# Kernel optimization log

Hardware: AMD Instinct MI355X
Metric: run time of the kernel (lower is better)

The kernel has to match this reference:

```python
import jax, jax.numpy as jnp
import numpy as np

R, S, V, F = 4096, 128, 3, 35  # n_rays, n_samples, n_views(=3 fixed by rgb_fc), in_feat_ch+3


def _kaiming(key, fan_out, fan_in):
    return jax.random.normal(key, (fan_out, fan_in), jnp.float32) * jnp.sqrt(2.0 / fan_in)


def setup_inputs() -> dict:
    key = jax.random.key(0)
    ks = jax.random.split(key, 8)
    rgb_feat = jax.random.normal(ks[0], (R, S, V, F), jnp.float32)
    # base_fc: 105 -> 64 -> 32
    bw1, bw2 = _kaiming(ks[1], 64, 105), _kaiming(ks[2], 32, 64)
    # vis_fc: 32 -> 32 -> 32
    vw1, vw2 = _kaiming(ks[3], 32, 32), _kaiming(ks[4], 32, 32)
    # rgb_fc: 96 -> 32 -> 16 -> 3
    rw1, rw2, rw3 = _kaiming(ks[5], 32, 96), _kaiming(ks[6], 16, 32), _kaiming(ks[7], 3, 16)
    z = jnp.zeros
    return {
        "rgb_feat": rgb_feat,
        "bw1": bw1, "bb1": z((64,)), "bw2": bw2, "bb2": z((32,)),
        "vw1": vw1, "vb1": z((32,)), "vw2": vw2, "vb2": z((32,)),
        "rw1": rw1, "rb1": z((32,)), "rw2": rw2, "rb2": z((16,)), "rw3": rw3, "rb3": z((3,)),
    }


def _lin(x, w, b):
    return x @ w.T + b


def reference(rgb_feat, bw1, bb1, bw2, bb2, vw1, vb1, vw2, vb2,
              rw1, rb1, rw2, rb2, rw3, rb3):
    elu = jax.nn.elu
    num_views = rgb_feat.shape[2]
    rgb_in = rgb_feat[..., :3]
    # fused mean/variance over the views axis (dim=2)
    mean = jnp.mean(rgb_feat, axis=2, keepdims=True)          # [R,S,1,F]
    var = jnp.mean((rgb_feat - mean) ** 2, axis=2, keepdims=True)
    globalfeat = jnp.concatenate([mean, var], axis=-1)         # [R,S,1,2F]
    x = jnp.concatenate(
        [jnp.broadcast_to(globalfeat, (rgb_feat.shape[0], rgb_feat.shape[1], num_views, globalfeat.shape[-1])),
         rgb_feat], axis=-1)                                   # [R,S,V,3F]
    x = elu(_lin(elu(_lin(x, bw1, bb1)), bw2, bb2))            # [R,S,V,32]
    x_vis = elu(_lin(elu(_lin(x / num_views, vw1, vb1)), vw2, vb2))
    x = x + x_vis
    h = x.reshape(x.shape[0], x.shape[1], num_views * 32)      # [R,S,96]
    rgb_out = jax.nn.sigmoid(_lin(elu(_lin(elu(_lin(h, rw1, rb1)), rw2, rb2)), rw3, rb3))
    return (rgb_in, rgb_out)
```

## Files before the change

kernel.cpp:

```cpp
#include <hip/hip_runtime.h>
#include <hip/hip_bf16.h>

#define NPTS      524288
#define OUT2_BASE 4718592

using bf16x8 = __attribute__((ext_vector_type(8))) short;
using f32x4  = __attribute__((ext_vector_type(4))) float;


__device__ __forceinline__ ushort f2bf(float f) {
    union { float f; unsigned u; } v; v.f = f;
    unsigned u = v.u;
    unsigned r = u + 0x7fffu + ((u >> 16) & 1u);
    return (ushort)(r >> 16);
}
__device__ __forceinline__ uint pack2(float a, float b) {
    union { __hip_bfloat162 h; uint u; } cv;
    cv.h = __float22bfloat162_rn(make_float2(a, b));
    return cv.u;
}
__device__ __forceinline__ float eluf(float x) {
    return fmaxf(x, 0.f) + __expf(fminf(x, 0.f)) - 1.f;
}
__device__ __forceinline__ float sigm(float x) { return 1.f / (1.f + __expf(-x)); }

__device__ __forceinline__ void load8(const float* __restrict__ p, float* d) {
    __builtin_memcpy(d, p, 16);
    __builtin_memcpy(d + 4, p + 4, 16);
}

__global__ void prep_k(const float* __restrict__ bw1, const float* __restrict__ bw2,
                       const float* __restrict__ vw1, const float* __restrict__ vw2,
                       const float* __restrict__ rw1, const float* __restrict__ rw2,
                       ushort* __restrict__ w)
{
    int i = blockIdx.x * 256 + threadIdx.x;
    if (i < 6144) {
        int n = i / 96, k = i % 96;
        float val = 0.f;
        if (k < 35)                 val = bw1[n * 105 + k];
        else if (k >= 40 && k < 75) val = bw1[n * 105 + 35 + (k - 40)];
        w[i] = f2bf(val);
    } else if (i < 10752) {
        int t = i - 6144, n = t / 72, k = t % 72;
        w[i] = f2bf(k < 35 ? bw1[n * 105 + 70 + k] : 0.f);
    } else if (i < 13056) {
        int t = i - 10752, n = t / 72, k = t % 72;
        w[i] = f2bf(k < 64 ? bw2[n * 64 + k] : 0.f);
    } else if (i < 14336) {
        int t = i - 13056, n = t / 40, k = t % 40;
        w[i] = f2bf(k < 32 ? vw1[n * 32 + k] * (1.f / 3.f) : 0.f);
    } else if (i < 15616) {
        int t = i - 14336, n = t / 40, k = t % 40;
        w[i] = f2bf(k < 32 ? vw2[n * 32 + k] : 0.f);
    } else if (i < 18944) {
        int t = i - 15616, n = t / 104, k = t % 104;
        w[i] = f2bf(k < 96 ? rw1[n * 96 + k] : 0.f);
    } else if (i < 19584) {
        int t = i - 18944, n = t / 40, k = t % 40;
        w[i] = f2bf(k < 32 ? rw2[n * 32 + k] : 0.f);
    }
}

__global__ __launch_bounds__(128, 4) void mlp_k(
    const float* __restrict__ feat, const ushort* __restrict__ w,
    const float* __restrict__ bb1, const float* __restrict__ bb2,
    const float* __restrict__ vb1, const float* __restrict__ vb2,
    const float* __restrict__ rb1, const float* __restrict__ rb2,
    const float* __restrict__ rw3, const float* __restrict__ rb3,
    float* __restrict__ out)
{
    __shared__ __align__(16) ushort shA[3456];
    __shared__ __align__(16) ushort shB[1664];
    __shared__ __align__(16) ushort shC[3456];

    const int tid  = threadIdx.x;
    const int wv   = tid >> 6;
    const int lane = tid & 63;
    const int n16  = lane & 15;
    const int quad = lane >> 4;
    const long long pbase = (long long)blockIdx.x * 16;

    const ushort* WG = w;
    const ushort* WF = w + 6144;
    const ushort* W2 = w + 10752;
    const ushort* V1 = w + 13056;
    const ushort* V2 = w + 14336;
    const ushort* R1 = w + 15616;
    const ushort* R2 = w + 18944;

    float bb1v[2];
#pragma unroll
    for (int ntl = 0; ntl < 2; ++ntl) bb1v[ntl] = bb1[(wv * 2 + ntl) * 16 + n16];
    const float bb2v = bb2[wv * 16 + n16];
    const float vb1v = vb1[wv * 16 + n16];
    const float vb2v = vb2[wv * 16 + n16];
    const float rb1v = rb1[wv * 16 + n16];
    const float rb2v = rb2[n16];

    {
        const uint4 z = make_uint4(0u, 0u, 0u, 0u);
        uint4* zc = (uint4*)shC;
        for (int i = tid; i < 144; i += 128) {
            int r = i / 3, c = i - r * 3;
            zc[r * 9 + 5 + c] = z;
        }
        if (tid < 32) {
            uint4* zb = (uint4*)shB;
            int r = tid >> 1, c = tid & 1;
            zb[r * 12 + 10 + c] = z;
        }
        for (int i = tid; i < 144; i += 128) {
            int p = i / 9, r = i - p * 9, v = r / 3, c = r - v * 3;
            out[pbase * 9 + i] = feat[(pbase + p) * 105 + v * 35 + c];
        }
        if (tid < 80) {
            int p  = tid / 5;
            int g  = tid - p * 5;
            int k8 = g * 8;
            const float* row = feat + (pbase + p) * 105;
            float X0[8], X1[8], X2[8];
            load8(row + k8,      X0);
            load8(row + 35 + k8, X1);
            if (k8 == 32 && (pbase + p) == (long long)NPTS - 1) {
                X2[0] = row[102]; X2[1] = row[103]; X2[2] = row[104];
                X2[3] = 0.f; X2[4] = 0.f; X2[5] = 0.f; X2[6] = 0.f; X2[7] = 0.f;
            } else {
                load8(row + 70 + k8, X2);
            }
            float M[8], VV[8];
#pragma unroll
            for (int j = 0; j < 8; ++j) {
                float a = X0[j], b = X1[j], c = X2[j];
                float m  = (a + b + c) * (1.f / 3.f);
                float da = a - m, db = b - m, dc = c - m;
                M[j]  = m;
                VV[j] = (da * da + db * db + dc * dc) * (1.f / 3.f);
            }
            *(uint4*)(shC + p * 72 + k8) =
                make_uint4(pack2(X0[0], X0[1]), pack2(X0[2], X0[3]),
                           pack2(X0[4], X0[5]), pack2(X0[6], X0[7]));
            *(uint4*)(shC + (16 + p) * 72 + k8) =
                make_uint4(pack2(X1[0], X1[1]), pack2(X1[2], X1[3]),
                           pack2(X1[4], X1[5]), pack2(X1[6], X1[7]));
            *(uint4*)(shC + (32 + p) * 72 + k8) =
                make_uint4(pack2(X2[0], X2[1]), pack2(X2[2], X2[3]),
                           pack2(X2[4], X2[5]), pack2(X2[6], X2[7]));
            *(uint4*)(shB + p * 96 + k8) =
                make_uint4(pack2(M[0], M[1]), pack2(M[2], M[3]),
                           pack2(M[4], M[5]), pack2(M[6], M[7]));
            *(uint4*)(shB + p * 96 + 40 + k8) =
                make_uint4(pack2(VV[0], VV[1]), pack2(VV[2], VV[3]),
                           pack2(VV[4], VV[5]), pack2(VV[6], VV[7]));
        }
    }
    __syncthreads();

    const f32x4 Z = {0.f, 0.f, 0.f, 0.f};

    f32x4 Cg[2]    = {Z, Z};
    f32x4 Cf[3][2] = {{Z, Z}, {Z, Z}, {Z, Z}};
#pragma unroll
    for (int ks = 0; ks < 3; ++ks) {
        bf16x8 a = *(const bf16x8*)(shB + n16 * 96 + ks * 32 + quad * 8);
#pragma unroll
        for (int ntl = 0; ntl < 2; ++ntl) {
            bf16x8 b = *(const bf16x8*)(WG + ((wv * 2 + ntl) * 16 + n16) * 96 + ks * 32 + quad * 8);
            Cg[ntl] = __builtin_amdgcn_mfma_f32_16x16x32_bf16(a, b, Cg[ntl], 0, 0, 0);
        }
    }
#pragma unroll
    for (int ks = 0; ks < 2; ++ks) {
        bf16x8 a0 = *(const bf16x8*)(shC + (0 * 16 + n16) * 72 + ks * 32 + quad * 8);
        bf16x8 a1 = *(const bf16x8*)(shC + (1 * 16 + n16) * 72 + ks * 32 + quad * 8);
        bf16x8 a2 = *(const bf16x8*)(shC + (2 * 16 + n16) * 72 + ks * 32 + quad * 8);
#pragma unroll
        for (int ntl = 0; ntl < 2; ++ntl) {
            bf16x8 b = *(const bf16x8*)(WF + ((wv * 2 + ntl) * 16 + n16) * 72 + ks * 32 + quad * 8);
            Cf[0][ntl] = __builtin_amdgcn_mfma_f32_16x16x32_bf16(a0, b, Cf[0][ntl], 0, 0, 0);
            Cf[1][ntl] = __builtin_amdgcn_mfma_f32_16x16x32_bf16(a1, b, Cf[1][ntl], 0, 0, 0);
            Cf[2][ntl] = __builtin_amdgcn_mfma_f32_16x16x32_bf16(a2, b, Cf[2][ntl], 0, 0, 0);
        }
    }
#pragma unroll
    for (int mt = 0; mt < 3; ++mt)
#pragma unroll
        for (int ntl = 0; ntl < 2; ++ntl) {
            float e0 = eluf(Cf[mt][ntl][0] + Cg[ntl][0] + bb1v[ntl]);
            float e1 = eluf(Cf[mt][ntl][1] + Cg[ntl][1] + bb1v[ntl]);
            float e2 = eluf(Cf[mt][ntl][2] + Cg[ntl][2] + bb1v[ntl]);
            float e3 = eluf(Cf[mt][ntl][3] + Cg[ntl][3] + bb1v[ntl]);
            int col = (wv * 2 + ntl) * 16 + n16;
            int r0  = (mt * 16 + quad * 4) * 72 + col;
            uint u01 = pack2(e0, e1), u23 = pack2(e2, e3);
            shA[r0]           = (ushort)u01;
            shA[r0 + 72]      = (ushort)(u01 >> 16);
            shA[r0 + 144]     = (ushort)u23;
            shA[r0 + 216]     = (ushort)(u23 >> 16);
        }
    __syncthreads();

    f32x4 C2[3] = {Z, Z, Z};
#pragma unroll
    for (int ks = 0; ks < 2; ++ks) {
        bf16x8 a0 = *(const bf16x8*)(shA + (0 * 16 + n16) * 72 + ks * 32 + quad * 8);
        bf16x8 a1 = *(const bf16x8*)(shA + (1 * 16 + n16) * 72 + ks * 32 + quad * 8);
        bf16x8 a2 = *(const bf16x8*)(shA + (2 * 16 + n16) * 72 + ks * 32 + quad * 8);
        bf16x8 b  = *(const bf16x8*)(W2 + (wv * 16 + n16) * 72 + ks * 32 + quad * 8);
        C2[0] = __builtin_amdgcn_mfma_f32_16x16x32_bf16(a0, b, C2[0], 0, 0, 0);
        C2[1] = __builtin_amdgcn_mfma_f32_16x16x32_bf16(a1, b, C2[1], 0, 0, 0);
        C2[2] = __builtin_amdgcn_mfma_f32_16x16x32_bf16(a2, b, C2[2], 0, 0, 0);
    }
    float h2r[3][4];
#pragma unroll
    for (int mt = 0; mt < 3; ++mt) {
        float e0 = eluf(C2[mt][0] + bb2v);
        float e1 = eluf(C2[mt][1] + bb2v);
        float e2 = eluf(C2[mt][2] + bb2v);
        float e3 = eluf(C2[mt][3] + bb2v);
        h2r[mt][0] = e0; h2r[mt][1] = e1; h2r[mt][2] = e2; h2r[mt][3] = e3;
        int r0 = (mt * 16 + quad * 4) * 72 + wv * 16 + n16;
        uint u01 = pack2(e0, e1), u23 = pack2(e2, e3);
        shC[r0]       = (ushort)u01;
        shC[r0 + 72]  = (ushort)(u01 >> 16);
        shC[r0 + 144] = (ushort)u23;
        shC[r0 + 216] = (ushort)(u23 >> 16);
    }
    __syncthreads();

    f32x4 T1[3] = {Z, Z, Z};
    {
        bf16x8 a0 = *(const bf16x8*)(shC + (0 * 16 + n16) * 72 + quad * 8);
        bf16x8 a1 = *(const bf16x8*)(shC + (1 * 16 + n16) * 72 + quad * 8);
        bf16x8 a2 = *(const bf16x8*)(shC + (2 * 16 + n16) * 72 + quad * 8);
        bf16x8 b  = *(const bf16x8*)(V1 + (wv * 16 + n16) * 40 + quad * 8);
        T1[0] = __builtin_amdgcn_mfma_f32_16x16x32_bf16(a0, b, T1[0], 0, 0, 0);
        T1[1] = __builtin_amdgcn_mfma_f32_16x16x32_bf16(a1, b, T1[1], 0, 0, 0);
        T1[2] = __builtin_amdgcn_mfma_f32_16x16x32_bf16(a2, b, T1[2], 0, 0, 0);
    }
#pragma unroll
    for (int mt = 0; mt < 3; ++mt) {
        float e0 = eluf(T1[mt][0] + vb1v);
        float e1 = eluf(T1[mt][1] + vb1v);
        float e2 = eluf(T1[mt][2] + vb1v);
        float e3 = eluf(T1[mt][3] + vb1v);
        int r0 = (mt * 16 + quad * 4) * 72 + wv * 16 + n16;
        uint u01 = pack2(e0, e1), u23 = pack2(e2, e3);
        shA[r0]       = (ushort)u01;
        shA[r0 + 72]  = (ushort)(u01 >> 16);
        shA[r0 + 144] = (ushort)u23;
        shA[r0 + 216] = (ushort)(u23 >> 16);
    }
    __syncthreads();

    f32x4 T2[3] = {Z, Z, Z};
    {
        bf16x8 a0 = *(const bf16x8*)(shA + (0 * 16 + n16) * 72 + quad * 8);
        bf16x8 a1 = *(const bf16x8*)(shA + (1 * 16 + n16) * 72 + quad * 8);
        bf16x8 a2 = *(const bf16x8*)(shA + (2 * 16 + n16) * 72 + quad * 8);
        bf16x8 b  = *(const bf16x8*)(V2 + (wv * 16 + n16) * 40 + quad * 8);
        T2[0] = __builtin_amdgcn_mfma_f32_16x16x32_bf16(a0, b, T2[0], 0, 0, 0);
        T2[1] = __builtin_amdgcn_mfma_f32_16x16x32_bf16(a1, b, T2[1], 0, 0, 0);
        T2[2] = __builtin_amdgcn_mfma_f32_16x16x32_bf16(a2, b, T2[2], 0, 0, 0);
    }
#pragma unroll
    for (int mt = 0; mt < 3; ++mt) {
        float x0  = h2r[mt][0] + eluf(T2[mt][0] + vb2v);
        float x1  = h2r[mt][1] + eluf(T2[mt][1] + vb2v);
        float x2v = h2r[mt][2] + eluf(T2[mt][2] + vb2v);
        float x3  = h2r[mt][3] + eluf(T2[mt][3] + vb2v);
        int col = mt * 32 + wv * 16 + n16;
        int r0  = (quad * 4) * 104 + col;
        uint u01 = pack2(x0, x1), u23 = pack2(x2v, x3);
        shB[r0]       = (ushort)u01;
        shB[r0 + 104] = (ushort)(u01 >> 16);
        shB[r0 + 208] = (ushort)u23;
        shB[r0 + 312] = (ushort)(u23 >> 16);
    }
    __syncthreads();

    f32x4 CR = Z;
#pragma unroll
    for (int ks = 0; ks < 3; ++ks) {
        bf16x8 a = *(const bf16x8*)(shB + n16 * 104 + ks * 32 + quad * 8);
        bf16x8 b = *(const bf16x8*)(R1 + (wv * 16 + n16) * 104 + ks * 32 + quad * 8);
        CR = __builtin_amdgcn_mfma_f32_16x16x32_bf16(a, b, CR, 0, 0, 0);
    }
    {
        float e0 = eluf(CR[0] + rb1v);
        float e1 = eluf(CR[1] + rb1v);
        float e2 = eluf(CR[2] + rb1v);
        float e3 = eluf(CR[3] + rb1v);
        int r0 = (quad * 4) * 40 + wv * 16 + n16;
        uint u01 = pack2(e0, e1), u23 = pack2(e2, e3);
        shC[r0]       = (ushort)u01;
        shC[r0 + 40]  = (ushort)(u01 >> 16);
        shC[r0 + 80]  = (ushort)u23;
        shC[r0 + 120] = (ushort)(u23 >> 16);
    }
    __syncthreads();

    f32x4 C3 = Z;
    {
        bf16x8 a = *(const bf16x8*)(shC + n16 * 40 + quad * 8);
        bf16x8 b = *(const bf16x8*)(R2 + n16 * 40 + quad * 8);
        C3 = __builtin_amdgcn_mfma_f32_16x16x32_bf16(a, b, C3, 0, 0, 0);
    }
    {
        float* r2b = (float*)shA;
#pragma unroll
        for (int rr = 0; rr < 2; ++rr) {
            int r = 2 * wv + rr;
            r2b[(quad * 4 + r) * 20 + n16] = eluf(C3[r] + rb2v);
        }
    }
    __syncthreads();

    if (tid < 48) {
        const float* r2b = (const float*)shA;
        int p = tid / 3, c = tid - p * 3;
        const float4* rr = (const float4*)(r2b + p * 20);
        const float4* w3 = (const float4*)(rw3 + c * 16);
        float4 a0 = rr[0], a1 = rr[1], a2 = rr[2], a3 = rr[3];
        float4 q0 = w3[0], q1 = w3[1], q2 = w3[2], q3 = w3[3];
        float s = rb3[c];
        s += a0.x * q0.x + a0.y * q0.y + a0.z * q0.z + a0.w * q0.w;
        s += a1.x * q1.x + a1.y * q1.y + a1.z * q1.z + a1.w * q1.w;
        s += a2.x * q2.x + a2.y * q2.y + a2.z * q2.z + a2.w * q2.w;
        s += a3.x * q3.x + a3.y * q3.y + a3.z * q3.z + a3.w * q3.w;
        out[OUT2_BASE + pbase * 3 + tid] = sigm(s);
    }
}

extern "C" void kernel_launch(void* const* d_in, const int* in_sizes, int n_in,
                              void* d_out, int out_size, void* d_ws, size_t ws_size,
                              hipStream_t stream) {
    const float* feat = (const float*)d_in[0];
    const float* bw1  = (const float*)d_in[1];
    const float* bb1  = (const float*)d_in[2];
    const float* bw2  = (const float*)d_in[3];
    const float* bb2  = (const float*)d_in[4];
    const float* vw1  = (const float*)d_in[5];
    const float* vb1  = (const float*)d_in[6];
    const float* vw2  = (const float*)d_in[7];
    const float* vb2  = (const float*)d_in[8];
    const float* rw1  = (const float*)d_in[9];
    const float* rb1  = (const float*)d_in[10];
    const float* rw2  = (const float*)d_in[11];
    const float* rb2  = (const float*)d_in[12];
    const float* rw3  = (const float*)d_in[13];
    const float* rb3  = (const float*)d_in[14];
    ushort* w  = (ushort*)d_ws;
    float* out = (float*)d_out;

    hipLaunchKernelGGL(prep_k, dim3(77), dim3(256), 0, stream,
                       bw1, bw2, vw1, vw2, rw1, rw2, w);
    hipLaunchKernelGGL(mlp_k, dim3(NPTS / 16), dim3(128), 0, stream,
                       feat, w, bb1, bb2, vb1, vb2, rb1, rb2, rw3, rb3, out);
}
```

Before: 429.0 us.

## Loop each block over many point tiles with weights held in registers

After: 484.0 us. 1.13x slower.

```diff
diff --git a/kernel.cpp b/kernel.cpp
--- a/kernel.cpp
+++ b/kernel.cpp
@@ -3,6 +3,9 @@
 
 #define NPTS      524288
 #define OUT2_BASE 4718592
+#define NTILES    32768
+#define NBLK      2048
+#define TPB       16
 
 using bf16x8 = __attribute__((ext_vector_type(8))) short;
 using f32x4  = __attribute__((ext_vector_type(4))) float;
@@ -79,7 +82,6 @@
     const int lane = tid & 63;
     const int n16  = lane & 15;
     const int quad = lane >> 4;
-    const long long pbase = (long long)blockIdx.x * 16;
 
     const ushort* WG = w;
     const ushort* WF = w + 6144;
@@ -98,6 +100,50 @@
     const float rb1v = rb1[wv * 16 + n16];
     const float rb2v = rb2[n16];
 
+    bf16x8 WFf[2][2], W2f[2];
+#pragma unroll
+    for (int ks = 0; ks < 2; ++ks) {
+#pragma unroll
+        for (int ntl = 0; ntl < 2; ++ntl)
+            WFf[ks][ntl] = *(const bf16x8*)(WF + ((wv * 2 + ntl) * 16 + n16) * 72 + ks * 32 + quad * 8);
+        W2f[ks] = *(const bf16x8*)(W2 + (wv * 16 + n16) * 72 + ks * 32 + quad * 8);
+    }
+    const bf16x8 V1f = *(const bf16x8*)(V1 + (wv * 16 + n16) * 40 + quad * 8);
+    const bf16x8 V2f = *(const bf16x8*)(V2 + (wv * 16 + n16) * 40 + quad * 8);
+    const bf16x8 R2f = *(const bf16x8*)(R2 + n16 * 40 + quad * 8);
+    const ushort* WGp[2] = { WG + ((wv * 2 + 0) * 16 + n16) * 96 + quad * 8,
+                             WG + ((wv * 2 + 1) * 16 + n16) * 96 + quad * 8 };
+    const ushort* R1p    = R1 + (wv * 16 + n16) * 104 + quad * 8;
+
+    const int c_p = tid / 9, c_r = tid - c_p * 9;
+    const int c_v = c_r / 3, c_c = c_r - c_v * 3;
+    const int cp_in0 = c_p * 105 + c_v * 35 + c_c;
+    const int i2 = tid + 128;
+    const int d_p = i2 / 9, d_r = i2 - d_p * 9;
+    const int d_v = d_r / 3, d_c = d_r - d_v * 3;
+    const int cp_in1 = d_p * 105 + d_v * 35 + d_c;
+
+    const int  bp   = tid / 5;
+    const int  k8   = (tid - bp * 5) * 8;
+    const bool bthr = tid < 80;
+    const bool gthr = bthr && (k8 == 32) && (bp == 15) && (blockIdx.x == NBLK - 1);
+    ushort* const stXf0 = shC + bp * 72 + k8;
+    ushort* const stXf1 = shC + (16 + bp) * 72 + k8;
+    ushort* const stXf2 = shC + (32 + bp) * 72 + k8;
+    ushort* const stXg0 = shB + bp * 96 + k8;
+    ushort* const stXg1 = shB + bp * 96 + 40 + k8;
+
+    const bool fthr = tid < 48;
+    const int  fp = tid / 3, fc = tid - fp * 3;
+    float4 q0 = {0,0,0,0}, q1 = q0, q2 = q0, q3 = q0;
+    float  rb3c = 0.f;
+    if (fthr) {
+        const float4* w3 = (const float4*)(rw3 + fc * 16);
+        q0 = w3[0]; q1 = w3[1]; q2 = w3[2]; q3 = w3[3];
+        rb3c = rb3[fc];
+    }
+    const float* const r2row = (const float*)shA + fp * 20;
+
     {
         const uint4 z = make_uint4(0u, 0u, 0u, 0u);
         uint4* zc = (uint4*)shC;
@@ -110,23 +156,29 @@
             int r = tid >> 1, c = tid & 1;
             zb[r * 12 + 10 + c] = z;
         }
-        for (int i = tid; i < 144; i += 128) {
-            int p = i / 9, r = i - p * 9, v = r / 3, c = r - v * 3;
-            out[pbase * 9 + i] = feat[(pbase + p) * 105 + v * 35 + c];
-        }
-        if (tid < 80) {
-            int p  = tid / 5;
-            int g  = tid - p * 5;
-            int k8 = g * 8;
-            const float* row = feat + (pbase + p) * 105;
+    }
+
+    const long long pbase0 = (long long)blockIdx.x * (TPB * 16);
+    const float* fin  = feat + pbase0 * 105;
+    const float* brow = feat + (pbase0 + bp) * 105;
+    float*       orgb = out + pbase0 * 9;
+    float*       o2   = out + OUT2_BASE + pbase0 * 3;
+
+    const f32x4 Z = {0.f, 0.f, 0.f, 0.f};
+
+#pragma unroll 1
+    for (int it = 0; it < TPB; ++it) {
+        orgb[tid] = fin[cp_in0];
+        if (tid < 16) orgb[i2] = fin[cp_in1];
+        if (bthr) {
             float X0[8], X1[8], X2[8];
-            load8(row + k8,      X0);
-            load8(row + 35 + k8, X1);
-            if (k8 == 32 && (pbase + p) == (long long)NPTS - 1) {
-                X2[0] = row[102]; X2[1] = row[103]; X2[2] = row[104];
+            load8(brow + k8,      X0);
+            load8(brow + 35 + k8, X1);
+            if (gthr && it == TPB - 1) {
+                X2[0] = brow[102]; X2[1] = brow[103]; X2[2] = brow[104];
                 X2[3] = 0.f; X2[4] = 0.f; X2[5] = 0.f; X2[6] = 0.f; X2[7] = 0.f;
             } else {
-                load8(row + 70 + k8, X2);
+                load8(brow + 70 + k8, X2);
             }
             float M[8], VV[8];
 #pragma unroll
@@ -137,198 +189,187 @@
                 M[j]  = m;
                 VV[j] = (da * da + db * db + dc * dc) * (1.f / 3.f);
             }
-            *(uint4*)(shC + p * 72 + k8) =
-                make_uint4(pack2(X0[0], X0[1]), pack2(X0[2], X0[3]),
-                           pack2(X0[4], X0[5]), pack2(X0[6], X0[7]));
-            *(uint4*)(shC + (16 + p) * 72 + k8) =
-                make_uint4(pack2(X1[0], X1[1]), pack2(X1[2], X1[3]),
-                           pack2(X1[4], X1[5]), pack2(X1[6], X1[7]));
-            *(uint4*)(shC + (32 + p) * 72 + k8) =
-                make_uint4(pack2(X2[0], X2[1]), pack2(X2[2], X2[3]),
-                           pack2(X2[4], X2[5]), pack2(X2[6], X2[7]));
-            *(uint4*)(shB + p * 96 + k8) =
-                make_uint4(pack2(M[0], M[1]), pack2(M[2], M[3]),
-                           pack2(M[4], M[5]), pack2(M[6], M[7]));
-            *(uint4*)(shB + p * 96 + 40 + k8) =
-                make_uint4(pack2(VV[0], VV[1]), pack2(VV[2], VV[3]),
-                           pack2(VV[4], VV[5]), pack2(VV[6], VV[7]));
-        }
-    }
-    __syncthreads();
-
-    const f32x4 Z = {0.f, 0.f, 0.f, 0.f};
-
-    f32x4 Cg[2]    = {Z, Z};
-    f32x4 Cf[3][2] = {{Z, Z}, {Z, Z}, {Z, Z}};
-#pragma unroll
-    for (int ks = 0; ks < 3; ++ks) {
-        bf16x8 a = *(const bf16x8*)(shB + n16 * 96 + ks * 32 + quad * 8);
-#pragma unroll
-        for (int ntl = 0; ntl < 2; ++ntl) {
-            bf16x8 b = *(const bf16x8*)(WG + ((wv * 2 + ntl) * 16 + n16) * 96 + ks * 32 + quad * 8);
-            Cg[ntl] = __builtin_amdgcn_mfma_f32_16x16x32_bf16(a, b, Cg[ntl], 0, 0, 0);
-        }
-    }
-#pragma unroll
-    for (int ks = 0; ks < 2; ++ks) {
-        bf16x8 a0 = *(const bf16x8*)(shC + (0 * 16 + n16) * 72 + ks * 32 + quad * 8);
-        bf16x8 a1 = *(const bf16x8*)(shC + (1 * 16 + n16) * 72 + ks * 32 + quad * 8);
-        bf16x8 a2 = *(const bf16x8*)(shC + (2 * 16 + n16) * 72 + ks * 32 + quad * 8);
-#pragma unroll
-        for (int ntl = 0; ntl < 2; ++ntl) {
-            bf16x8 b = *(const bf16x8*)(WF + ((wv * 2 + ntl) * 16 + n16) * 72 + ks * 32 + quad * 8);
-            Cf[0][ntl] = __builtin_amdgcn_mfma_f32_16x16x32_bf16(a0, b, Cf[0][ntl], 0, 0, 0);
-            Cf[1][ntl] = __builtin_amdgcn_mfma_f32_16x16x32_bf16(a1, b, Cf[1][ntl], 0, 0, 0);
-            Cf[2][ntl] = __builtin_amdgcn_mfma_f32_16x16x32_bf16(a2, b, Cf[2][ntl], 0, 0, 0);
-        }
-    }
-#pragma unroll
-    for (int mt = 0; mt < 3; ++mt)
-#pragma unroll
-        for (int ntl = 0; ntl < 2; ++ntl) {
-            float e0 = eluf(Cf[mt][ntl][0] + Cg[ntl][0] + bb1v[ntl]);
-            float e1 = eluf(Cf[mt][ntl][1] + Cg[ntl][1] + bb1v[ntl]);
-            float e2 = eluf(Cf[mt][ntl][2] + Cg[ntl][2] + bb1v[ntl]);
-            float e3 = eluf(Cf[mt][ntl][3] + Cg[ntl][3] + bb1v[ntl]);
-            int col = (wv * 2 + ntl) * 16 + n16;
-            int r0  = (mt * 16 + quad * 4) * 72 + col;
+            *(uint4*)stXf0 = make_uint4(pack2(X0[0], X0[1]), pack2(X0[2], X0[3]),
+                                        pack2(X0[4], X0[5]), pack2(X0[6], X0[7]));
+            *(uint4*)stXf1 = make_uint4(pack2(X1[0], X1[1]), pack2(X1[2], X1[3]),
+                                        pack2(X1[4], X1[5]), pack2(X1[6], X1[7]));
+            *(uint4*)stXf2 = make_uint4(pack2(X2[0], X2[1]), pack2(X2[2], X2[3]),
+                                        pack2(X2[4], X2[5]), pack2(X2[6], X2[7]));
+            *(uint4*)stXg0 = make_uint4(pack2(M[0], M[1]), pack2(M[2], M[3]),
+                                        pack2(M[4], M[5]), pack2(M[6], M[7]));
+            *(uint4*)stXg1 = make_uint4(pack2(VV[0], VV[1]), pack2(VV[2], VV[3]),
+                                        pack2(VV[4], VV[5]), pack2(VV[6], VV[7]));
+        }
+        __syncthreads();
+
+        f32x4 Cg[2]    = {Z, Z};
+        f32x4 Cf[3][2] = {{Z, Z}, {Z, Z}, {Z, Z}};
+#pragma unroll
+        for (int ks = 0; ks < 3; ++ks) {
+            bf16x8 a = *(const bf16x8*)(shB + n16 * 96 + ks * 32 + quad * 8);
+#pragma unroll
+            for (int ntl = 0; ntl < 2; ++ntl) {
+                bf16x8 b = *(const bf16x8*)(WGp[ntl] + ks * 32);
+                Cg[ntl] = __builtin_amdgcn_mfma_f32_16x16x32_bf16(a, b, Cg[ntl], 0, 0, 0);
+            }
+        }
+#pragma unroll
+        for (int ks = 0; ks < 2; ++ks) {
+            bf16x8 a0 = *(const bf16x8*)(shC + (0 * 16 + n16) * 72 + ks * 32 + quad * 8);
+            bf16x8 a1 = *(const bf16x8*)(shC + (1 * 16 + n16) * 72 + ks * 32 + quad * 8);
+            bf16x8 a2 = *(const bf16x8*)(shC + (2 * 16 + n16) * 72 + ks * 32 + quad * 8);
+#pragma unroll
+            for (int ntl = 0; ntl < 2; ++ntl) {
+                Cf[0][ntl] = __builtin_amdgcn_mfma_f32_16x16x32_bf16(a0, WFf[ks][ntl], Cf[0][ntl], 0, 0, 0);
+                Cf[1][ntl] = __builtin_amdgcn_mfma_f32_16x16x32_bf16(a1, WFf[ks][ntl], Cf[1][ntl], 0, 0, 0);
+                Cf[2][ntl] = __builtin_amdgcn_mfma_f32_16x16x32_bf16(a2, WFf[ks][ntl], Cf[2][ntl], 0, 0, 0);
+            }
+        }
+#pragma unroll
+        for (int mt = 0; mt < 3; ++mt)
+#pragma unroll
+            for (int ntl = 0; ntl < 2; ++ntl) {
+                float e0 = eluf(Cf[mt][ntl][0] + Cg[ntl][0] + bb1v[ntl]);
+                float e1 = eluf(Cf[mt][ntl][1] + Cg[ntl][1] + bb1v[ntl]);
+                float e2 = eluf(Cf[mt][ntl][2] + Cg[ntl][2] + bb1v[ntl]);
+                float e3 = eluf(Cf[mt][ntl][3] + Cg[ntl][3] + bb1v[ntl]);
+                int col = (wv * 2 + ntl) * 16 + n16;
+                int r0  = (mt * 16 + quad * 4) * 72 + col;
+                uint u01 = pack2(e0, e1), u23 = pack2(e2, e3);
+                shA[r0]       = (ushort)u01;
+                shA[r0 + 72]  = (ushort)(u01 >> 16);
+                shA[r0 + 144] = (ushort)u23;
+                shA[r0 + 216] = (ushort)(u23 >> 16);
+            }
+        __syncthreads();
+
+        f32x4 C2[3] = {Z, Z, Z};
+#pragma unroll
+        for (int ks = 0; ks < 2; ++ks) {
+            bf16x8 a0 = *(const bf16x8*)(shA + (0 * 16 + n16) * 72 + ks * 32 + quad * 8);
+            bf16x8 a1 = *(const bf16x8*)(shA + (1 * 16 + n16) * 72 + ks * 32 + quad * 8);
+            bf16x8 a2 = *(const bf16x8*)(shA + (2 * 16 + n16) * 72 + ks * 32 + quad * 8);
+            C2[0] = __builtin_amdgcn_mfma_f32_16x16x32_bf16(a0, W2f[ks], C2[0], 0, 0, 0);
+            C2[1] = __builtin_amdgcn_mfma_f32_16x16x32_bf16(a1, W2f[ks], C2[1], 0, 0, 0);
+            C2[2] = __builtin_amdgcn_mfma_f32_16x16x32_bf16(a2, W2f[ks], C2[2], 0, 0, 0);
+        }
+        float h2r[3][4];
+#pragma unroll
+        for (int mt = 0; mt < 3; ++mt) {
+            float e0 = eluf(C2[mt][0] + bb2v);
+            float e1 = eluf(C2[mt][1] + bb2v);
+            float e2 = eluf(C2[mt][2] + bb2v);
+            float e3 = eluf(C2[mt][3] + bb2v);
+            h2r[mt][0] = e0; h2r[mt][1] = e1; h2r[mt][2] = e2; h2r[mt][3] = e3;
+            int r0 = (mt * 16 + quad * 4) * 72 + wv * 16 + n16;
             uint u01 = pack2(e0, e1), u23 = pack2(e2, e3);
-            shA[r0]           = (ushort)u01;
-            shA[r0 + 72]      = (ushort)(u01 >> 16);
-            shA[r0 + 144]     = (ushort)u23;
-            shA[r0 + 216]     = (ushort)(u23 >> 16);
-        }
-    __syncthreads();
-
-    f32x4 C2[3] = {Z, Z, Z};
-#pragma unroll
-    for (int ks = 0; ks < 2; ++ks) {
-        bf16x8 a0 = *(const bf16x8*)(shA + (0 * 16 + n16) * 72 + ks * 32 + quad * 8);
-        bf16x8 a1 = *(const bf16x8*)(shA + (1 * 16 + n16) * 72 + ks * 32 + quad * 8);
-        bf16x8 a2 = *(const bf16x8*)(shA + (2 * 16 + n16) * 72 + ks * 32 + quad * 8);
-        bf16x8 b  = *(const bf16x8*)(W2 + (wv * 16 + n16) * 72 + ks * 32 + quad * 8);
-        C2[0] = __builtin_amdgcn_mfma_f32_16x16x32_bf16(a0, b, C2[0], 0, 0, 0);
-        C2[1] = __builtin_amdgcn_mfma_f32_16x16x32_bf16(a1, b, C2[1], 0, 0, 0);
-        C2[2] = __builtin_amdgcn_mfma_f32_16x16x32_bf16(a2, b, C2[2], 0, 0, 0);
-    }
-    float h2r[3][4];
-#pragma unroll
-    for (int mt = 0; mt < 3; ++mt) {
-        float e0 = eluf(C2[mt][0] + bb2v);
-        float e1 = eluf(C2[mt][1] + bb2v);
-        float e2 = eluf(C2[mt][2] + bb2v);
-        float e3 = eluf(C2[mt][3] + bb2v);
-        h2r[mt][0] = e0; h2r[mt][1] = e1; h2r[mt][2] = e2; h2r[mt][3] = e3;
-        int r0 = (mt * 16 + quad * 4) * 72 + wv * 16 + n16;
-        uint u01 = pack2(e0, e1), u23 = pack2(e2, e3);
-        shC[r0]       = (ushort)u01;
-        shC[r0 + 72]  = (ushort)(u01 >> 16);
-        shC[r0 + 144] = (ushort)u23;
-        shC[r0 + 216] = (ushort)(u23 >> 16);
-    }
-    __syncthreads();
-
-    f32x4 T1[3] = {Z, Z, Z};
-    {
-        bf16x8 a0 = *(const bf16x8*)(shC + (0 * 16 + n16) * 72 + quad * 8);
-        bf16x8 a1 = *(const bf16x8*)(shC + (1 * 16 + n16) * 72 + quad * 8);
-        bf16x8 a2 = *(const bf16x8*)(shC + (2 * 16 + n16) * 72 + quad * 8);
-        bf16x8 b  = *(const bf16x8*)(V1 + (wv * 16 + n16) * 40 + quad * 8);
-        T1[0] = __builtin_amdgcn_mfma_f32_16x16x32_bf16(a0, b, T1[0], 0, 0, 0);
-        T1[1] = __builtin_amdgcn_mfma_f32_16x16x32_bf16(a1, b, T1[1], 0, 0, 0);
-        T1[2] = __builtin_amdgcn_mfma_f32_16x16x32_bf16(a2, b, T1[2], 0, 0, 0);
-    }
-#pragma unroll
-    for (int mt = 0; mt < 3; ++mt) {
-        float e0 = eluf(T1[mt][0] + vb1v);
-        float e1 = eluf(T1[mt][1] + vb1v);
-        float e2 = eluf(T1[mt][2] + vb1v);
-        float e3 = eluf(T1[mt][3] + vb1v);
-        int r0 = (mt * 16 + quad * 4) * 72 + wv * 16 + n16;
-        uint u01 = pack2(e0, e1), u23 = pack2(e2, e3);
-        shA[r0]       = (ushort)u01;
-        shA[r0 + 72]  = (ushort)(u01 >> 16);
-        shA[r0 + 144] = (ushort)u23;
-        shA[r0 + 216] = (ushort)(u23 >> 16);
-    }
-    __syncthreads();
-
-    f32x4 T2[3] = {Z, Z, Z};
-    {
-        bf16x8 a0 = *(const bf16x8*)(shA + (0 * 16 + n16) * 72 + quad * 8);
-        bf16x8 a1 = *(const bf16x8*)(shA + (1 * 16 + n16) * 72 + quad * 8);
-        bf16x8 a2 = *(const bf16x8*)(shA + (2 * 16 + n16) * 72 + quad * 8);
-        bf16x8 b  = *(const bf16x8*)(V2 + (wv * 16 + n16) * 40 + quad * 8);
-        T2[0] = __builtin_amdgcn_mfma_f32_16x16x32_bf16(a0, b, T2[0], 0, 0, 0);
-        T2[1] = __builtin_amdgcn_mfma_f32_16x16x32_bf16(a1, b, T2[1], 0, 0, 0);
-        T2[2] = __builtin_amdgcn_mfma_f32_16x16x32_bf16(a2, b, T2[2], 0, 0, 0);
-    }
-#pragma unroll
-    for (int mt = 0; mt < 3; ++mt) {
-        float x0  = h2r[mt][0] + eluf(T2[mt][0] + vb2v);
-        float x1  = h2r[mt][1] + eluf(T2[mt][1] + vb2v);
-        float x2v = h2r[mt][2] + eluf(T2[mt][2] + vb2v);
-        float x3  = h2r[mt][3] + eluf(T2[mt][3] + vb2v);
-        int col = mt * 32 + wv * 16 + n16;
-        int r0  = (quad * 4) * 104 + col;
-        uint u01 = pack2(x0, x1), u23 = pack2(x2v, x3);
-        shB[r0]       = (ushort)u01;
-        shB[r0 + 104] = (ushort)(u01 >> 16);
-        shB[r0 + 208] = (ushort)u23;
-        shB[r0 + 312] = (ushort)(u23 >> 16);
-    }
-    __syncthreads();
-
-    f32x4 CR = Z;
-#pragma unroll
-    for (int ks = 0; ks < 3; ++ks) {
-        bf16x8 a = *(const bf16x8*)(shB + n16 * 104 + ks * 32 + quad * 8);
-        bf16x8 b = *(const bf16x8*)(R1 + (wv * 16 + n16) * 104 + ks * 32 + quad * 8);
-        CR = __builtin_amdgcn_mfma_f32_16x16x32_bf16(a, b, CR, 0, 0, 0);
-    }
-    {
-        float e0 = eluf(CR[0] + rb1v);
-        float e1 = eluf(CR[1] + rb1v);
-        float e2 = eluf(CR[2] + rb1v);
-        float e3 = eluf(CR[3] + rb1v);
-        int r0 = (quad * 4) * 40 + wv * 16 + n16;
-        uint u01 = pack2(e0, e1), u23 = pack2(e2, e3);
-        shC[r0]       = (ushort)u01;
-        shC[r0 + 40]  = (ushort)(u01 >> 16);
-        shC[r0 + 80]  = (ushort)u23;
-        shC[r0 + 120] = (ushort)(u23 >> 16);
-    }
-    __syncthreads();
-
-    f32x4 C3 = Z;
-    {
-        bf16x8 a = *(const bf16x8*)(shC + n16 * 40 + quad * 8);
-        bf16x8 b = *(const bf16x8*)(R2 + n16 * 40 + quad * 8);
-        C3 = __builtin_amdgcn_mfma_f32_16x16x32_bf16(a, b, C3, 0, 0, 0);
-    }
-    {
-        float* r2b = (float*)shA;
-#pragma unroll
-        for (int rr = 0; rr < 2; ++rr) {
-            int r = 2 * wv + rr;
-            r2b[(quad * 4 + r) * 20 + n16] = eluf(C3[r] + rb2v);
-        }
-    }
-    __syncthreads();
-
-    if (tid < 48) {
-        const float* r2b = (const float*)shA;
-        int p = tid / 3, c = tid - p * 3;
-        const float4* rr = (const float4*)(r2b + p * 20);
-        const float4* w3 = (const float4*)(rw3 + c * 16);
-        float4 a0 = rr[0], a1 = rr[1], a2 = rr[2], a3 = rr[3];
-        float4 q0 = w3[0], q1 = w3[1], q2 = w3[2], q3 = w3[3];
-        float s = rb3[c];
-        s += a0.x * q0.x + a0.y * q0.y + a0.z * q0.z + a0.w * q0.w;
-        s += a1.x * q1.x + a1.y * q1.y + a1.z * q1.z + a1.w * q1.w;
-        s += a2.x * q2.x + a2.y * q2.y + a2.z * q2.z + a2.w * q2.w;
-        s += a3.x * q3.x + a3.y * q3.y + a3.z * q3.z + a3.w * q3.w;
-        out[OUT2_BASE + pbase * 3 + tid] = sigm(s);
+            shC[r0]       = (ushort)u01;
+            shC[r0 + 72]  = (ushort)(u01 >> 16);
+            shC[r0 + 144] = (ushort)u23;
+            shC[r0 + 216] = (ushort)(u23 >> 16);
+        }
+        __syncthreads();
+
+        f32x4 T1[3] = {Z, Z, Z};
+        {
+            bf16x8 a0 = *(const bf16x8*)(shC + (0 * 16 + n16) * 72 + quad * 8);
+            bf16x8 a1 = *(const bf16x8*)(shC + (1 * 16 + n16) * 72 + quad * 8);
+            bf16x8 a2 = *(const bf16x8*)(shC + (2 * 16 + n16) * 72 + quad * 8);
+            T1[0] = __builtin_amdgcn_mfma_f32_16x16x32_bf16(a0, V1f, T1[0], 0, 0, 0);
+            T1[1] = __builtin_amdgcn_mfma_f32_16x16x32_bf16(a1, V1f, T1[1], 0, 0, 0);
+            T1[2] = __builtin_amdgcn_mfma_f32_16x16x32_bf16(a2, V1f, T1[2], 0, 0, 0);
+        }
+#pragma unroll
+        for (int mt = 0; mt < 3; ++mt) {
+            float e0 = eluf(T1[mt][0] + vb1v);
+            float e1 = eluf(T1[mt][1] + vb1v);
+            float e2 = eluf(T1[mt][2] + vb1v);
+            float e3 = eluf(T1[mt][3] + vb1v);
+            int r0 = (mt * 16 + quad * 4) * 72 + wv * 16 + n16;
+            uint u01 = pack2(e0, e1), u23 = pack2(e2, e3);
+            shA[r0]       = (ushort)u01;
+            shA[r0 + 72]  = (ushort)(u01 >> 16);
+            shA[r0 + 144] = (ushort)u23;
+            shA[r0 + 216] = (ushort)(u23 >> 16);
+        }
+        __syncthreads();
+
+        f32x4 T2[3] = {Z, Z, Z};
+        {
+            bf16x8 a0 = *(const bf16x8*)(shA + (0 * 16 + n16) * 72 + quad * 8);
+            bf16x8 a1 = *(const bf16x8*)(shA + (1 * 16 + n16) * 72 + quad * 8);
+            bf16x8 a2 = *(const bf16x8*)(shA + (2 * 16 + n16) * 72 + quad * 8);
+            T2[0] = __builtin_amdgcn_mfma_f32_16x16x32_bf16(a0, V2f, T2[0], 0, 0, 0);
+            T2[1] = __builtin_amdgcn_mfma_f32_16x16x32_bf16(a1, V2f, T2[1], 0, 0, 0);
+            T2[2] = __builtin_amdgcn_mfma_f32_16x16x32_bf16(a2, V2f, T2[2], 0, 0, 0);
+        }
+#pragma unroll
+        for (int mt = 0; mt < 3; ++mt) {
+            float x0  = h2r[mt][0] + eluf(T2[mt][0] + vb2v);
+            float x1  = h2r[mt][1] + eluf(T2[mt][1] + vb2v);
+            float x2v = h2r[mt][2] + eluf(T2[mt][2] + vb2v);
+            float x3  = h2r[mt][3] + eluf(T2[mt][3] + vb2v);
+            int col = mt * 32 + wv * 16 + n16;
+            int r0  = (quad * 4) * 104 + col;
+            uint u01 = pack2(x0, x1), u23 = pack2(x2v, x3);
+            shB[r0]       = (ushort)u01;
+            shB[r0 + 104] = (ushort)(u01 >> 16);
+            shB[r0 + 208] = (ushort)u23;
+            shB[r0 + 312] = (ushort)(u23 >> 16);
+        }
+        __syncthreads();
+
+        f32x4 CR = Z;
+#pragma unroll
+        for (int ks = 0; ks < 3; ++ks) {
+            bf16x8 a = *(const bf16x8*)(shB + n16 * 104 + ks * 32 + quad * 8);
+            bf16x8 b = *(const bf16x8*)(R1p + ks * 32);
+            CR = __builtin_amdgcn_mfma_f32_16x16x32_bf16(a, b, CR, 0, 0, 0);
+        }
+        {
+            float e0 = eluf(CR[0] + rb1v);
+            float e1 = eluf(CR[1] + rb1v);
+            float e2 = eluf(CR[2] + rb1v);
+            float e3 = eluf(CR[3] + rb1v);
+            int r0 = (quad * 4) * 40 + wv * 16 + n16;
+            uint u01 = pack2(e0, e1), u23 = pack2(e2, e3);
+            shC[r0]       = (ushort)u01;
+            shC[r0 + 40]  = (ushort)(u01 >> 16);
+            shC[r0 + 80]  = (ushort)u23;
+            shC[r0 + 120] = (ushort)(u23 >> 16);
+        }
+        __syncthreads();
+
+        f32x4 C3 = Z;
+        {
+            bf16x8 a = *(const bf16x8*)(shC + n16 * 40 + quad * 8);
+            C3 = __builtin_amdgcn_mfma_f32_16x16x32_bf16(a, R2f, C3, 0, 0, 0);
+        }
+        {
+            float* r2b = (float*)shA;
+#pragma unroll
+            for (int rr = 0; rr < 2; ++rr) {
+                int r = 2 * wv + rr;
+                r2b[(quad * 4 + r) * 20 + n16] = eluf(C3[r] + rb2v);
+            }
+        }
+        __syncthreads();
+
+        if (fthr) {
+            const float4* rr = (const float4*)r2row;
+            float4 a0 = rr[0], a1 = rr[1], a2 = rr[2], a3 = rr[3];
+            float s = rb3c;
+            s += a0.x * q0.x + a0.y * q0.y + a0.z * q0.z + a0.w * q0.w;
+            s += a1.x * q1.x + a1.y * q1.y + a1.z * q1.z + a1.w * q1.w;
+            s += a2.x * q2.x + a2.y * q2.y + a2.z * q2.z + a2.w * q2.w;
+            s += a3.x * q3.x + a3.y * q3.y + a3.z * q3.z + a3.w * q3.w;
+            o2[tid] = sigm(s);
+        }
+
+        fin  += 16 * 105;
+        brow += 16 * 105;
+        orgb += 144;
+        o2   += 48;
     }
 }
 
@@ -355,6 +396,6 @@
 
     hipLaunchKernelGGL(prep_k, dim3(77), dim3(256), 0, stream,
                        bw1, bw2, vw1, vw2, rw1, rw2, w);
-    hipLaunchKernelGGL(mlp_k, dim3(NPTS / 16), dim3(128), 0, stream,
+    hipLaunchKernelGGL(mlp_k, dim3(NBLK), dim3(128), 0, stream,
                        feat, w, bb1, bb2, vb1, vb2, rb1, rb2, rw3, rb3, out);
 }
```
